# Performance work log

Measured on AMD Instinct MI355X. Metric: run time of the kernel, lower is better.

## Reference

```python
import jax, jax.numpy as jnp
import numpy as np

IN_FEATURES = 4096
OUT_FEATURES = 4096
N_TOKENS = 4096  # batch*seq rows fed through the linear layer


def setup_inputs() -> dict:
    key = jax.random.key(0)
    kx, kw, kb = jax.random.split(key, 3)
    x = jax.random.normal(kx, (N_TOKENS, IN_FEATURES), dtype=jnp.float32)
    # kaiming_uniform-like init scale for weight, uniform bias as in reset_parameters
    bound_w = float(np.sqrt(6.0 / ((1.0 + 5.0) * IN_FEATURES)))  # kaiming_uniform a=sqrt(5)
    weight = jax.random.uniform(kw, (OUT_FEATURES, IN_FEATURES), dtype=jnp.float32,
                                minval=-bound_w, maxval=bound_w)
    bound_b = float(1.0 / np.sqrt(IN_FEATURES))
    bias = jax.random.uniform(kb, (OUT_FEATURES,), dtype=jnp.float32,
                              minval=-bound_b, maxval=bound_b)
    return {"x": x, "weight": weight, "bias": bias}


def reference(x, weight, bias):
    # quantize_weights(bits=8): scale = 127 / max|W|; W_int8 = int8-cast(W*scale)
    # (numpy int8 cast truncates toward zero). The cutlass int8 GEMM computes
    # x_int8 @ W_int8^T, dequantized by 1/scale, plus bias. Math equivalent:
    # y = x @ (trunc(W*scale)/scale)^T + bias
    scale = 127.0 / jnp.max(jnp.abs(weight))
    w_q = jnp.clip(jnp.trunc(weight * scale), -127.0, 127.0)  # emulated int8 weight
    w_deq = w_q / scale                                       # [out, in]
    return jnp.einsum('ti,oi->to', x, w_deq) + bias           # [tokens, out]
```

## Files before the change

### kernel.cpp

```cpp
#include <hip/hip_runtime.h>
#include <stdint.h>

#define M_DIM 4096
#define N_DIM 4096
#define K_DIM 4096

typedef int i32x4 __attribute__((ext_vector_type(4)));

__global__ void maxabs_kernel(const float* __restrict__ w,
                              unsigned int* __restrict__ out_bits, int n4) {
    __shared__ float sred[4];
    int tid = blockIdx.x * blockDim.x + threadIdx.x;
    int stride = gridDim.x * blockDim.x;
    const float4* w4 = (const float4*)w;
    float m = 0.f;
    for (int i = tid; i < n4; i += stride) {
        float4 a = w4[i];
        m = fmaxf(m, fmaxf(fmaxf(fabsf(a.x), fabsf(a.y)), fmaxf(fabsf(a.z), fabsf(a.w))));
    }
    for (int off = 32; off > 0; off >>= 1) m = fmaxf(m, __shfl_xor(m, off));
    if ((threadIdx.x & 63) == 0) sred[threadIdx.x >> 6] = m;
    __syncthreads();
    if (threadIdx.x == 0) {
        m = fmaxf(fmaxf(sred[0], sred[1]), fmaxf(sred[2], sred[3]));
        atomicMax(out_bits, __float_as_uint(m));
    }
}

__global__ void quantfuse_kernel(const float* __restrict__ w,
                                 const float* __restrict__ x,
                                 const unsigned int* __restrict__ mb,
                                 int* __restrict__ wq4,
                                 char* __restrict__ xq,
                                 float* __restrict__ xsinv, int n4) {
    __shared__ float sred[4];
    if (blockIdx.x < 4096) {
        const int row = blockIdx.x;
        const int t = threadIdx.x;
        const float4* xr = (const float4*)(x + (size_t)row * K_DIM);
        float4 v[4];
        float m = 0.f;
        #pragma unroll
        for (int i = 0; i < 4; ++i) {
            v[i] = xr[t * 4 + i];
            m = fmaxf(m, fmaxf(fmaxf(fabsf(v[i].x), fabsf(v[i].y)),
                               fmaxf(fabsf(v[i].z), fabsf(v[i].w))));
        }
        for (int off = 32; off > 0; off >>= 1) m = fmaxf(m, __shfl_xor(m, off));
        if ((t & 63) == 0) sred[t >> 6] = m;
        __syncthreads();
        m = fmaxf(fmaxf(fmaxf(sred[0], sred[1]), fmaxf(sred[2], sred[3])), 1e-30f);
        if (t == 0) xsinv[row] = m * (1.0f / 127.0f);
        const float scale = 127.0f / m;
        int4 o;
        int* op = (int*)&o;
        #pragma unroll
        for (int i = 0; i < 4; ++i) {
            int a = (int)rintf(v[i].x * scale);
            int b = (int)rintf(v[i].y * scale);
            int c = (int)rintf(v[i].z * scale);
            int d = (int)rintf(v[i].w * scale);
            op[i] = (a & 0xff) | ((b & 0xff) << 8) | ((c & 0xff) << 16) | (d << 24);
        }
        *(int4*)(xq + (size_t)row * K_DIM + t * 16) = o;
    } else {
        const float wscale = 127.0f / __uint_as_float(mb[0]);
        int tid = (blockIdx.x - 4096) * blockDim.x + threadIdx.x;
        const int stride = 2048 * 256;
        const float4* w4 = (const float4*)w;
        for (int i = tid; i < n4; i += stride) {
            float4 a = w4[i];
            int w0 = (int)fminf(fmaxf(truncf(a.x * wscale), -127.f), 127.f);
            int w1 = (int)fminf(fmaxf(truncf(a.y * wscale), -127.f), 127.f);
            int w2 = (int)fminf(fmaxf(truncf(a.z * wscale), -127.f), 127.f);
            int w3 = (int)fminf(fmaxf(truncf(a.w * wscale), -127.f), 127.f);
            wq4[i] = (w0 & 0xff) | ((w1 & 0xff) << 8) | ((w2 & 0xff) << 16) | (w3 << 24);
        }
    }
}

#define BAR()   __builtin_amdgcn_s_barrier()
#define FENCE() __builtin_amdgcn_sched_barrier(0)

#define MFMA_I8(ACC, AF, BF) \
    asm("v_mfma_i32_16x16x64_i8 %0, %1, %2, %0" : "+v"(ACC) : "v"(AF), "v"(BF))

__global__ __launch_bounds__(512, 2) void gemm_i8(
    const char* __restrict__ A,
    const char* __restrict__ B,
    const unsigned int* __restrict__ mb,
    const float* __restrict__ xsinv,
    const float* __restrict__ bias,
    float* __restrict__ C)
{
    __shared__ __align__(16) char sM[131072];

    int bid = (blockIdx.x & 7) * 32 + (blockIdx.x >> 3);
    const int bm = bid >> 4;
    const int bn = bid & 15;

    const int t    = threadIdx.x;
    const int wave = t >> 6;
    const int lane = t & 63;
    const int wm   = wave >> 2;
    const int wn   = wave & 3;

    i32x4 acc[2][2][4][2] = {};

    const int chunk = (((lane >> 4) << 4) ^ ((lane & 7) << 4));
    const int lbA0 = ((lane & 15) << 7) + chunk + wm * 8192;
    const int lbA1 = lbA0 ^ 64;
    const int lbB0 = ((lane & 15) << 7) + chunk + wn * 4096 + 65536;
    const int lbB1 = lbB0 ^ 64;

    const int srow = t >> 3;
    const int cch  = (t & 7) ^ (srow & 7);
    const char* Abase = A + (size_t)(bm * 256 + srow) * K_DIM + cch * 16;
    const char* Bbase = B + (size_t)(bn * 256 + srow) * K_DIM + cch * 16;
    const int wave_lds = wave * 1024;

#define STAGE(SRC, REG, H, KT, BUF) do {                                                \
        const char* _s = SRC + (H) * (128 * K_DIM) + ((KT) << 7);                       \
        char* _d = sM + (REG) + (BUF) * 32768 + (H) * 16384 + wave_lds;                 \
        __builtin_amdgcn_global_load_lds(                                               \
            (const __attribute__((address_space(1))) void*)_s,                          \
            (__attribute__((address_space(3))) void*)_d, 16, 0, 0);                     \
        __builtin_amdgcn_global_load_lds(                                               \
            (const __attribute__((address_space(1))) void*)(_s + (size_t)64 * K_DIM),   \
            (__attribute__((address_space(3))) void*)(_d + 8192), 16, 0, 0);            \
    } while(0)

#define LDA(H, BUF, AF) do {                                                            \
        _Pragma("unroll") for (int mi = 0; mi < 4; ++mi) {                              \
            AF[mi][0] = *(const i32x4*)(sM + (BUF)*32768 + (H)*16384 + mi*2048 + lbA0); \
            AF[mi][1] = *(const i32x4*)(sM + (BUF)*32768 + (H)*16384 + mi*2048 + lbA1); \
        }                                                                               \
    } while(0)

#define LDB(G, BUF, BF) do {                                                            \
        _Pragma("unroll") for (int ni = 0; ni < 2; ++ni) {                              \
            BF[ni][0] = *(const i32x4*)(sM + (BUF)*32768 + (G)*16384 + ni*2048 + lbB0); \
            BF[ni][1] = *(const i32x4*)(sM + (BUF)*32768 + (G)*16384 + ni*2048 + lbB1); \
        }                                                                               \
    } while(0)

#define MMAQ(H, G, AF, BF)                                                              \
        _Pragma("unroll") for (int kk = 0; kk < 2; ++kk)                                \
        _Pragma("unroll") for (int mi = 0; mi < 4; ++mi)                                \
        _Pragma("unroll") for (int ni = 0; ni < 2; ++ni)                                \
            MFMA_I8(acc[H][G][mi][ni], AF[mi][kk], BF[ni][kk]);

#define TILE(BUF, OBUF, KN) do {                                                        \
        LDA(0, BUF, af0); LDB(0, BUF, bf0);                    \
        FENCE();                                                                        \
        LDB(1, BUF, bf1);                                                  \
        STAGE(Abase, 0,     0, KN, OBUF);                                               \
        STAGE(Bbase, 65536, 0, KN, OBUF);                                               \
        STAGE(Abase, 0,     1, KN, OBUF);                                               \
        STAGE(Bbase, 65536, 1, KN, OBUF);                                               \
        LDA(1, BUF, af1);                                                  \
        FENCE();                                                                        \
        __builtin_amdgcn_s_setprio(1);                                                  \
        MMAQ(0, 0, af0, bf0);                                                           \
        MMAQ(0, 1, af0, bf1);                                                           \
        MMAQ(1, 1, af1, bf1);                                                           \
        MMAQ(1, 0, af1, bf0);                                                           \
        __builtin_amdgcn_s_setprio(0);                                                  \
        asm volatile("s_waitcnt vmcnt(0)");      \
        BAR();                                                                          \
        FENCE();                                                                        \
    } while(0)

    STAGE(Abase, 0,     0, 0, 0);
    STAGE(Bbase, 65536, 0, 0, 0);
    STAGE(Abase, 0,     1, 0, 0);
    STAGE(Bbase, 65536, 1, 0, 0);
    asm volatile("s_waitcnt vmcnt(0)");
    BAR();
    FENCE();

    i32x4 af0[4][2], af1[4][2], bf0[2][2], bf1[2][2];

    for (int it = 0; it < 16; ++it) {
        TILE(0, 1, (2 * it + 1) & 31);
        TILE(1, 0, (2 * it + 2) & 31);
    }

    const float wdq = __uint_as_float(mb[0]) * (1.0f / 127.0f);

    #pragma unroll
    for (int h = 0; h < 2; ++h)
    #pragma unroll
    for (int mi = 0; mi < 4; ++mi) {
        const int grow0 = bm * 256 + h * 128 + wm * 64 + mi * 16 + (lane >> 4) * 4;
        float rs[4];
        #pragma unroll
        for (int rg = 0; rg < 4; ++rg) rs[rg] = xsinv[grow0 + rg] * wdq;
        #pragma unroll
        for (int g = 0; g < 2; ++g)
        #pragma unroll
        for (int ni = 0; ni < 2; ++ni) {
            const int gcol = bn * 256 + g * 128 + wn * 32 + ni * 16 + (lane & 15);
            const float bv = bias[gcol];
            #pragma unroll
            for (int rg = 0; rg < 4; ++rg)
                C[(size_t)(grow0 + rg) * N_DIM + gcol] =
                    (float)acc[h][g][mi][ni][rg] * rs[rg] + bv;
        }
    }

#undef STAGE
#undef LDA
#undef LDB
#undef MMAQ
#undef TILE
}

extern "C" void kernel_launch(void* const* d_in, const int* in_sizes, int n_in,
                              void* d_out, int out_size, void* d_ws, size_t ws_size,
                              hipStream_t stream) {
    const float* x    = (const float*)d_in[0];
    const float* w    = (const float*)d_in[1];
    const float* bias = (const float*)d_in[2];
    float* out = (float*)d_out;

    unsigned int* maxbits = (unsigned int*)d_ws;
    float* xsinv = (float*)((char*)d_ws + 256);
    char*  xq    = (char*)d_ws + 32768;
    char*  wq    = (char*)d_ws + 32768 + (size_t)M_DIM * K_DIM;

    hipMemsetAsync(d_ws, 0, 8, stream);

    const int n4 = (N_DIM * K_DIM) / 4;
    maxabs_kernel<<<1024, 256, 0, stream>>>(w, maxbits, n4);
    quantfuse_kernel<<<4096 + 2048, 256, 0, stream>>>(w, x, maxbits, (int*)wq, xq, xsinv, n4);

    const int grid = (M_DIM / 256) * (N_DIM / 256);
    gemm_i8<<<grid, 512, 0, stream>>>(xq, wq, maxbits, xsinv, bias, out);
}
```

Measured before the change: 114.4 us.

## Load A fragments directly from global memory and halve GEMM shared memory

The GEMM stops staging the activation (A) tile through LDS and has each wave load its A fragments straight from global memory into registers, so only B is double-buffered in LDS and the shared allocation drops from 128KB to 64KB. The intent is to reduce LDS traffic and pressure and free LDS capacity. In exchange, A loads become uncoalesced per-row global reads with no software prefetch, issued at the start of each tile and stalled on before the MFMAs. The prep kernels are also reorganised: the x quantisation now runs alongside the weight max reduction, and weight quantisation moves to its own launch after them.

```diff
diff --git a/kernel.cpp b/kernel.cpp
--- a/kernel.cpp
+++ b/kernel.cpp
@@ -7,32 +7,11 @@
 
 typedef int i32x4 __attribute__((ext_vector_type(4)));
 
-__global__ void maxabs_kernel(const float* __restrict__ w,
-                              unsigned int* __restrict__ out_bits, int n4) {
-    __shared__ float sred[4];
-    int tid = blockIdx.x * blockDim.x + threadIdx.x;
-    int stride = gridDim.x * blockDim.x;
-    const float4* w4 = (const float4*)w;
-    float m = 0.f;
-    for (int i = tid; i < n4; i += stride) {
-        float4 a = w4[i];
-        m = fmaxf(m, fmaxf(fmaxf(fabsf(a.x), fabsf(a.y)), fmaxf(fabsf(a.z), fabsf(a.w))));
-    }
-    for (int off = 32; off > 0; off >>= 1) m = fmaxf(m, __shfl_xor(m, off));
-    if ((threadIdx.x & 63) == 0) sred[threadIdx.x >> 6] = m;
-    __syncthreads();
-    if (threadIdx.x == 0) {
-        m = fmaxf(fmaxf(sred[0], sred[1]), fmaxf(sred[2], sred[3]));
-        atomicMax(out_bits, __float_as_uint(m));
-    }
-}
-
-__global__ void quantfuse_kernel(const float* __restrict__ w,
-                                 const float* __restrict__ x,
-                                 const unsigned int* __restrict__ mb,
-                                 int* __restrict__ wq4,
-                                 char* __restrict__ xq,
-                                 float* __restrict__ xsinv, int n4) {
+__global__ void prep_kernel(const float* __restrict__ w,
+                            const float* __restrict__ x,
+                            unsigned int* __restrict__ out_bits,
+                            char* __restrict__ xq,
+                            float* __restrict__ xsinv) {
     __shared__ float sred[4];
     if (blockIdx.x < 4096) {
         const int row = blockIdx.x;
@@ -64,18 +43,39 @@
         }
         *(int4*)(xq + (size_t)row * K_DIM + t * 16) = o;
     } else {
-        const float wscale = 127.0f / __uint_as_float(mb[0]);
         int tid = (blockIdx.x - 4096) * blockDim.x + threadIdx.x;
-        const int stride = 2048 * 256;
+        const int stride = 1024 * 256;
+        const int n4 = (N_DIM * K_DIM) / 4;
         const float4* w4 = (const float4*)w;
+        float m = 0.f;
         for (int i = tid; i < n4; i += stride) {
             float4 a = w4[i];
-            int w0 = (int)fminf(fmaxf(truncf(a.x * wscale), -127.f), 127.f);
-            int w1 = (int)fminf(fmaxf(truncf(a.y * wscale), -127.f), 127.f);
-            int w2 = (int)fminf(fmaxf(truncf(a.z * wscale), -127.f), 127.f);
-            int w3 = (int)fminf(fmaxf(truncf(a.w * wscale), -127.f), 127.f);
-            wq4[i] = (w0 & 0xff) | ((w1 & 0xff) << 8) | ((w2 & 0xff) << 16) | (w3 << 24);
-        }
+            m = fmaxf(m, fmaxf(fmaxf(fabsf(a.x), fabsf(a.y)), fmaxf(fabsf(a.z), fabsf(a.w))));
+        }
+        for (int off = 32; off > 0; off >>= 1) m = fmaxf(m, __shfl_xor(m, off));
+        if ((threadIdx.x & 63) == 0) sred[threadIdx.x >> 6] = m;
+        __syncthreads();
+        if (threadIdx.x == 0) {
+            m = fmaxf(fmaxf(sred[0], sred[1]), fmaxf(sred[2], sred[3]));
+            atomicMax(out_bits, __float_as_uint(m));
+        }
+    }
+}
+
+__global__ void wquant_kernel(const float* __restrict__ w,
+                              const unsigned int* __restrict__ mb,
+                              int* __restrict__ wq4, int n4) {
+    const float wscale = 127.0f / __uint_as_float(mb[0]);
+    int tid = blockIdx.x * blockDim.x + threadIdx.x;
+    int stride = gridDim.x * blockDim.x;
+    const float4* w4 = (const float4*)w;
+    for (int i = tid; i < n4; i += stride) {
+        float4 a = w4[i];
+        int w0 = (int)fminf(fmaxf(truncf(a.x * wscale), -127.f), 127.f);
+        int w1 = (int)fminf(fmaxf(truncf(a.y * wscale), -127.f), 127.f);
+        int w2 = (int)fminf(fmaxf(truncf(a.z * wscale), -127.f), 127.f);
+        int w3 = (int)fminf(fmaxf(truncf(a.w * wscale), -127.f), 127.f);
+        wq4[i] = (w0 & 0xff) | ((w1 & 0xff) << 8) | ((w2 & 0xff) << 16) | (w3 << 24);
     }
 }
 
@@ -93,7 +93,7 @@
     const float* __restrict__ bias,
     float* __restrict__ C)
 {
-    __shared__ __align__(16) char sM[131072];
+    __shared__ __align__(16) char sM[65536];
 
     int bid = (blockIdx.x & 7) * 32 + (blockIdx.x >> 3);
     const int bm = bid >> 4;
@@ -108,20 +108,20 @@
     i32x4 acc[2][2][4][2] = {};
 
     const int chunk = (((lane >> 4) << 4) ^ ((lane & 7) << 4));
-    const int lbA0 = ((lane & 15) << 7) + chunk + wm * 8192;
-    const int lbA1 = lbA0 ^ 64;
-    const int lbB0 = ((lane & 15) << 7) + chunk + wn * 4096 + 65536;
+    const int lbB0 = ((lane & 15) << 7) + chunk + wn * 4096;
     const int lbB1 = lbB0 ^ 64;
 
     const int srow = t >> 3;
     const int cch  = (t & 7) ^ (srow & 7);
-    const char* Abase = A + (size_t)(bm * 256 + srow) * K_DIM + cch * 16;
     const char* Bbase = B + (size_t)(bn * 256 + srow) * K_DIM + cch * 16;
     const int wave_lds = wave * 1024;
 
-#define STAGE(SRC, REG, H, KT, BUF) do {                                                \
-        const char* _s = SRC + (H) * (128 * K_DIM) + ((KT) << 7);                       \
-        char* _d = sM + (REG) + (BUF) * 32768 + (H) * 16384 + wave_lds;                 \
+    const char* Agbase = A + (size_t)(bm * 256 + wm * 64 + (lane & 15)) * K_DIM
+                           + ((lane >> 4) << 4);
+
+#define STAGEB(H, KT, BUF) do {                                                         \
+        const char* _s = Bbase + (H) * (128 * K_DIM) + ((KT) << 7);                     \
+        char* _d = sM + (BUF) * 32768 + (H) * 16384 + wave_lds;                         \
         __builtin_amdgcn_global_load_lds(                                               \
             (const __attribute__((address_space(1))) void*)_s,                          \
             (__attribute__((address_space(3))) void*)_d, 16, 0, 0);                     \
@@ -130,10 +130,11 @@
             (__attribute__((address_space(3))) void*)(_d + 8192), 16, 0, 0);            \
     } while(0)
 
-#define LDA(H, BUF, AF) do {                                                            \
+#define LDAG(H, KT, AF) do {                                                            \
+        const char* _a = Agbase + (size_t)(H) * (128 * K_DIM) + ((KT) << 7);            \
         _Pragma("unroll") for (int mi = 0; mi < 4; ++mi) {                              \
-            AF[mi][0] = *(const i32x4*)(sM + (BUF)*32768 + (H)*16384 + mi*2048 + lbA0); \
-            AF[mi][1] = *(const i32x4*)(sM + (BUF)*32768 + (H)*16384 + mi*2048 + lbA1); \
+            AF[mi][0] = *(const i32x4*)(_a + mi * (16 * K_DIM));                        \
+            AF[mi][1] = *(const i32x4*)(_a + mi * (16 * K_DIM) + 64);                   \
         }                                                                               \
     } while(0)
 
@@ -150,15 +151,12 @@
         _Pragma("unroll") for (int ni = 0; ni < 2; ++ni)                                \
             MFMA_I8(acc[H][G][mi][ni], AF[mi][kk], BF[ni][kk]);
 
-#define TILE(BUF, OBUF, KN) do {                                                        \
-        LDA(0, BUF, af0); LDB(0, BUF, bf0);                    \
-        FENCE();                                                                        \
-        LDB(1, BUF, bf1);                                                  \
-        STAGE(Abase, 0,     0, KN, OBUF);                                               \
-        STAGE(Bbase, 65536, 0, KN, OBUF);                                               \
-        STAGE(Abase, 0,     1, KN, OBUF);                                               \
-        STAGE(Bbase, 65536, 1, KN, OBUF);                                               \
-        LDA(1, BUF, af1);                                                  \
+#define TILE(BUF, OBUF, TC, KN) do {                                                    \
+        LDAG(0, TC, af0);                                                   \
+        LDAG(1, TC, af1);                                                   \
+        LDB(0, BUF, bf0); LDB(1, BUF, bf1);                              \
+        STAGEB(0, KN, OBUF);                                                            \
+        STAGEB(1, KN, OBUF);                                           \
         FENCE();                                                                        \
         __builtin_amdgcn_s_setprio(1);                                                  \
         MMAQ(0, 0, af0, bf0);                                                           \
@@ -166,15 +164,14 @@
         MMAQ(1, 1, af1, bf1);                                                           \
         MMAQ(1, 0, af1, bf0);                                                           \
         __builtin_amdgcn_s_setprio(0);                                                  \
-        asm volatile("s_waitcnt vmcnt(0)");      \
+        FENCE();                                                                        \
+        asm volatile("s_waitcnt vmcnt(0)");       \
         BAR();                                                                          \
         FENCE();                                                                        \
     } while(0)
 
-    STAGE(Abase, 0,     0, 0, 0);
-    STAGE(Bbase, 65536, 0, 0, 0);
-    STAGE(Abase, 0,     1, 0, 0);
-    STAGE(Bbase, 65536, 1, 0, 0);
+    STAGEB(0, 0, 0);
+    STAGEB(1, 0, 0);
     asm volatile("s_waitcnt vmcnt(0)");
     BAR();
     FENCE();
@@ -182,8 +179,8 @@
     i32x4 af0[4][2], af1[4][2], bf0[2][2], bf1[2][2];
 
     for (int it = 0; it < 16; ++it) {
-        TILE(0, 1, (2 * it + 1) & 31);
-        TILE(1, 0, (2 * it + 2) & 31);
+        TILE(0, 1, (2 * it),     (2 * it + 1) & 31);
+        TILE(1, 0, (2 * it + 1), (2 * it + 2) & 31);
     }
 
     const float wdq = __uint_as_float(mb[0]) * (1.0f / 127.0f);
@@ -209,8 +206,8 @@
         }
     }
 
-#undef STAGE
-#undef LDA
+#undef STAGEB
+#undef LDAG
 #undef LDB
 #undef MMAQ
 #undef TILE
@@ -232,8 +229,8 @@
     hipMemsetAsync(d_ws, 0, 8, stream);
 
     const int n4 = (N_DIM * K_DIM) / 4;
-    maxabs_kernel<<<1024, 256, 0, stream>>>(w, maxbits, n4);
-    quantfuse_kernel<<<4096 + 2048, 256, 0, stream>>>(w, x, maxbits, (int*)wq, xq, xsinv, n4);
+    prep_kernel<<<4096 + 1024, 256, 0, stream>>>(w, x, maxbits, xq, xsinv);
+    wquant_kernel<<<2048, 256, 0, stream>>>(w, maxbits, (int*)wq, n4);
 
     const int grid = (M_DIM / 256) * (N_DIM / 256);
     gemm_i8<<<grid, 512, 0, stream>>>(xq, wq, maxbits, xsinv, bias, out);
```

Measured after the change: 209.5 us. +83.0%, slower.

## Restructure quantization prep: fuse weight max with x quant, drop memset and atomics

Applied to the files above, without the earlier changes.

The weight max-abs reduction now runs alongside activation quantization in one kernel, with each block writing a partial max instead of using a global atomicMax. A second kernel reduces the 2048 partials redundantly in every block and then quantizes the weights. This removes the memset launch and the atomics, and overlaps the x quantization with the weight reduction. The cost is each of the 2048 blocks re-reading the 8KB partial array, and x blocks now handle two rows each with extra barriers.

```diff
diff --git a/kernel.cpp b/kernel.cpp
--- a/kernel.cpp
+++ b/kernel.cpp
@@ -7,75 +7,91 @@
 
 typedef int i32x4 __attribute__((ext_vector_type(4)));
 
-__global__ void maxabs_kernel(const float* __restrict__ w,
-                              unsigned int* __restrict__ out_bits, int n4) {
+__global__ void prep1_kernel(const float* __restrict__ w,
+                             const float* __restrict__ x,
+                             float* __restrict__ wpmax,
+                             char* __restrict__ xq,
+                             float* __restrict__ xsinv) {
     __shared__ float sred[4];
-    int tid = blockIdx.x * blockDim.x + threadIdx.x;
-    int stride = gridDim.x * blockDim.x;
-    const float4* w4 = (const float4*)w;
-    float m = 0.f;
-    for (int i = tid; i < n4; i += stride) {
-        float4 a = w4[i];
-        m = fmaxf(m, fmaxf(fmaxf(fabsf(a.x), fabsf(a.y)), fmaxf(fabsf(a.z), fabsf(a.w))));
-    }
-    for (int off = 32; off > 0; off >>= 1) m = fmaxf(m, __shfl_xor(m, off));
-    if ((threadIdx.x & 63) == 0) sred[threadIdx.x >> 6] = m;
-    __syncthreads();
-    if (threadIdx.x == 0) {
-        m = fmaxf(fmaxf(sred[0], sred[1]), fmaxf(sred[2], sred[3]));
-        atomicMax(out_bits, __float_as_uint(m));
-    }
-}
-
-__global__ void quantfuse_kernel(const float* __restrict__ w,
-                                 const float* __restrict__ x,
-                                 const unsigned int* __restrict__ mb,
-                                 int* __restrict__ wq4,
-                                 char* __restrict__ xq,
-                                 float* __restrict__ xsinv, int n4) {
-    __shared__ float sred[4];
-    if (blockIdx.x < 4096) {
-        const int row = blockIdx.x;
-        const int t = threadIdx.x;
-        const float4* xr = (const float4*)(x + (size_t)row * K_DIM);
-        float4 v[4];
+    const int t = threadIdx.x;
+    if (blockIdx.x < 2048) {
+        int tid = blockIdx.x * 256 + t;
+        const int stride = 2048 * 256;
+        const int n4 = (N_DIM * K_DIM) / 4;
+        const float4* w4 = (const float4*)w;
         float m = 0.f;
-        #pragma unroll
-        for (int i = 0; i < 4; ++i) {
-            v[i] = xr[t * 4 + i];
-            m = fmaxf(m, fmaxf(fmaxf(fabsf(v[i].x), fabsf(v[i].y)),
-                               fmaxf(fabsf(v[i].z), fabsf(v[i].w))));
+        for (int i = tid; i < n4; i += stride) {
+            float4 a = w4[i];
+            m = fmaxf(m, fmaxf(fmaxf(fabsf(a.x), fabsf(a.y)), fmaxf(fabsf(a.z), fabsf(a.w))));
         }
         for (int off = 32; off > 0; off >>= 1) m = fmaxf(m, __shfl_xor(m, off));
         if ((t & 63) == 0) sred[t >> 6] = m;
         __syncthreads();
-        m = fmaxf(fmaxf(fmaxf(sred[0], sred[1]), fmaxf(sred[2], sred[3])), 1e-30f);
-        if (t == 0) xsinv[row] = m * (1.0f / 127.0f);
-        const float scale = 127.0f / m;
-        int4 o;
-        int* op = (int*)&o;
-        #pragma unroll
-        for (int i = 0; i < 4; ++i) {
-            int a = (int)rintf(v[i].x * scale);
-            int b = (int)rintf(v[i].y * scale);
-            int c = (int)rintf(v[i].z * scale);
-            int d = (int)rintf(v[i].w * scale);
-            op[i] = (a & 0xff) | ((b & 0xff) << 8) | ((c & 0xff) << 16) | (d << 24);
+        if (t == 0)
+            wpmax[blockIdx.x] = fmaxf(fmaxf(sred[0], sred[1]), fmaxf(sred[2], sred[3]));
+    } else {
+        const int rbase = (blockIdx.x - 2048) * 2;
+        #pragma unroll
+        for (int r = 0; r < 2; ++r) {
+            const int row = rbase + r;
+            const float4* xr = (const float4*)(x + (size_t)row * K_DIM);
+            float4 v[4];
+            float m = 0.f;
+            #pragma unroll
+            for (int i = 0; i < 4; ++i) {
+                v[i] = xr[t * 4 + i];
+                m = fmaxf(m, fmaxf(fmaxf(fabsf(v[i].x), fabsf(v[i].y)),
+                                   fmaxf(fabsf(v[i].z), fabsf(v[i].w))));
+            }
+            for (int off = 32; off > 0; off >>= 1) m = fmaxf(m, __shfl_xor(m, off));
+            if ((t & 63) == 0) sred[t >> 6] = m;
+            __syncthreads();
+            m = fmaxf(fmaxf(fmaxf(sred[0], sred[1]), fmaxf(sred[2], sred[3])), 1e-30f);
+            if (t == 0) xsinv[row] = m * (1.0f / 127.0f);
+            const float scale = 127.0f / m;
+            int4 o;
+            int* op = (int*)&o;
+            #pragma unroll
+            for (int i = 0; i < 4; ++i) {
+                int a = (int)rintf(v[i].x * scale);
+                int b = (int)rintf(v[i].y * scale);
+                int c = (int)rintf(v[i].z * scale);
+                int d = (int)rintf(v[i].w * scale);
+                op[i] = (a & 0xff) | ((b & 0xff) << 8) | ((c & 0xff) << 16) | (d << 24);
+            }
+            *(int4*)(xq + (size_t)row * K_DIM + t * 16) = o;
+            __syncthreads();
         }
-        *(int4*)(xq + (size_t)row * K_DIM + t * 16) = o;
-    } else {
-        const float wscale = 127.0f / __uint_as_float(mb[0]);
-        int tid = (blockIdx.x - 4096) * blockDim.x + threadIdx.x;
-        const int stride = 2048 * 256;
-        const float4* w4 = (const float4*)w;
-        for (int i = tid; i < n4; i += stride) {
-            float4 a = w4[i];
-            int w0 = (int)fminf(fmaxf(truncf(a.x * wscale), -127.f), 127.f);
-            int w1 = (int)fminf(fmaxf(truncf(a.y * wscale), -127.f), 127.f);
-            int w2 = (int)fminf(fmaxf(truncf(a.z * wscale), -127.f), 127.f);
-            int w3 = (int)fminf(fmaxf(truncf(a.w * wscale), -127.f), 127.f);
-            wq4[i] = (w0 & 0xff) | ((w1 & 0xff) << 8) | ((w2 & 0xff) << 16) | (w3 << 24);
-        }
+    }
+}
+
+__global__ void prep2_kernel(const float* __restrict__ w,
+                             const float* __restrict__ wpmax,
+                             int* __restrict__ wq4,
+                             float* __restrict__ wdq_out) {
+    __shared__ float sred[4];
+    const int t = threadIdx.x;
+    float m = 0.f;
+    #pragma unroll
+    for (int i = 0; i < 8; ++i) m = fmaxf(m, wpmax[t * 8 + i]);
+    for (int off = 32; off > 0; off >>= 1) m = fmaxf(m, __shfl_xor(m, off));
+    if ((t & 63) == 0) sred[t >> 6] = m;
+    __syncthreads();
+    const float maxv = fmaxf(fmaxf(sred[0], sred[1]), fmaxf(sred[2], sred[3]));
+    const float wscale = 127.0f / maxv;
+    if (blockIdx.x == 0 && t == 0) *wdq_out = maxv * (1.0f / 127.0f);
+
+    int tid = blockIdx.x * 256 + t;
+    const int stride = 2048 * 256;
+    const int n4 = (N_DIM * K_DIM) / 4;
+    const float4* w4 = (const float4*)w;
+    for (int i = tid; i < n4; i += stride) {
+        float4 a = w4[i];
+        int w0 = (int)fminf(fmaxf(truncf(a.x * wscale), -127.f), 127.f);
+        int w1 = (int)fminf(fmaxf(truncf(a.y * wscale), -127.f), 127.f);
+        int w2 = (int)fminf(fmaxf(truncf(a.z * wscale), -127.f), 127.f);
+        int w3 = (int)fminf(fmaxf(truncf(a.w * wscale), -127.f), 127.f);
+        wq4[i] = (w0 & 0xff) | ((w1 & 0xff) << 8) | ((w2 & 0xff) << 16) | (w3 << 24);
     }
 }
 
@@ -88,7 +104,7 @@
 __global__ __launch_bounds__(512, 2) void gemm_i8(
     const char* __restrict__ A,
     const char* __restrict__ B,
-    const unsigned int* __restrict__ mb,
+    const float* __restrict__ wdqp,
     const float* __restrict__ xsinv,
     const float* __restrict__ bias,
     float* __restrict__ C)
@@ -166,7 +182,7 @@
         MMAQ(1, 1, af1, bf1);                                                           \
         MMAQ(1, 0, af1, bf0);                                                           \
         __builtin_amdgcn_s_setprio(0);                                                  \
-        asm volatile("s_waitcnt vmcnt(0)");      \
+        asm volatile("s_waitcnt vmcnt(0)");              \
         BAR();                                                                          \
         FENCE();                                                                        \
     } while(0)
@@ -186,7 +202,7 @@
         TILE(1, 0, (2 * it + 2) & 31);
     }
 
-    const float wdq = __uint_as_float(mb[0]) * (1.0f / 127.0f);
+    const float wdq = *wdqp;
 
     #pragma unroll
     for (int h = 0; h < 2; ++h)
@@ -224,17 +240,15 @@
     const float* bias = (const float*)d_in[2];
     float* out = (float*)d_out;
 
-    unsigned int* maxbits = (unsigned int*)d_ws;
-    float* xsinv = (float*)((char*)d_ws + 256);
+    float* wpmax = (float*)d_ws;
+    float* wdqp  = (float*)((char*)d_ws + 8192);
+    float* xsinv = (float*)((char*)d_ws + 8448);
     char*  xq    = (char*)d_ws + 32768;
     char*  wq    = (char*)d_ws + 32768 + (size_t)M_DIM * K_DIM;
 
-    hipMemsetAsync(d_ws, 0, 8, stream);
-
-    const int n4 = (N_DIM * K_DIM) / 4;
-    maxabs_kernel<<<1024, 256, 0, stream>>>(w, maxbits, n4);
-    quantfuse_kernel<<<4096 + 2048, 256, 0, stream>>>(w, x, maxbits, (int*)wq, xq, xsinv, n4);
+    prep1_kernel<<<4096, 256, 0, stream>>>(w, x, wpmax, xq, xsinv);
+    prep2_kernel<<<2048, 256, 0, stream>>>(w, wpmax, (int*)wq, wdqp);
 
     const int grid = (M_DIM / 256) * (N_DIM / 256);
-    gemm_i8<<<grid, 512, 0, stream>>>(xq, wq, maxbits, xsinv, bias, out);
-}
+    gemm_i8<<<grid, 512, 0, stream>>>(xq, wq, wdqp, xsinv, bias, out);
+}
```

After: 101.1 us, median of 2. -11.7%, faster.
